# Performance work log

Measured on AMD Instinct MI355X. Metric: run time of the kernel, lower is better.

Reference implementation:

```python
import jax, jax.numpy as jnp
import numpy as np

ALPHA = 8.3  # depth-similarity decay from Depth-aware CNN
K = 3        # kernel size
PAD = 1      # padding (stride=1, dilation=1)


def _patches(x, k, pad):
    """Extract kxk stride-1 patches. x: (B,C,H,W) -> (B,C,k,k,H,W)."""
    B, C, H, W = x.shape
    xp = jnp.pad(x, ((0, 0), (0, 0), (pad, pad), (pad, pad)))
    rows = []
    for i in range(k):
        cols = [xp[:, :, i:i + H, j:j + W] for j in range(k)]
        rows.append(jnp.stack(cols, axis=2))          # (B,C,k,H,W)
    return jnp.stack(rows, axis=2)                     # (B,C,k,k,H,W)


def setup_inputs() -> dict:
    key = jax.random.key(0)
    k1, k2, k3 = jax.random.split(key, 3)
    B, Cin, H, W = 8, 512, 64, 64
    Cout = 64
    x = jax.random.normal(k1, (B, Cin, H, W), dtype=jnp.float32)
    depth = jax.random.uniform(k2, (B, 1, H, W), dtype=jnp.float32)
    stdv = 1.0 / np.sqrt(Cin * K * K)
    weight = jax.random.uniform(k3, (Cout, Cin, K, K), dtype=jnp.float32,
                                minval=-stdv, maxval=stdv)
    return {"input": x, "depth": depth, "weight": weight}


def reference(input, depth, weight):
    # depth-modulated conv: out(p0) = sum_pn w(pn) * x(p0+pn) * exp(-a*|d(p0)-d(p0+pn)|)
    xpat = _patches(input, K, PAD)                 # (B,Cin,K,K,H,W)
    dpat = _patches(depth, K, PAD)                 # (B,1,K,K,H,W)
    d0 = depth[:, :, None, None, :, :]             # center depth (B,1,1,1,H,W)
    gate = jnp.exp(-ALPHA * jnp.abs(d0 - dpat))    # (B,1,K,K,H,W)
    out = jnp.einsum('ocij,bcijhw->bohw', weight, xpat * gate)
    return out
```

## Files before the change

kernel.cpp:

```cpp
#include <hip/hip_runtime.h>
#include <math.h>

#define ALPHA 8.3f
#define XSZ   8448
#define WSZ   18432
#define BUFSZ 26880

typedef short v8s  __attribute__((ext_vector_type(8)));
typedef float v16f __attribute__((ext_vector_type(16)));
typedef float v4f  __attribute__((ext_vector_type(4)));

static __device__ __forceinline__ unsigned short f2bf(float f) {
    unsigned int u = __float_as_uint(f);
    u = (u + 0x7fffu + ((u >> 16) & 1u)) >> 16;
    return (unsigned short)u;
}

static __device__ __forceinline__ void async16(const void* g, void* l) {
    __builtin_amdgcn_global_load_lds(
        (const __attribute__((address_space(1))) unsigned int*)g,
        (__attribute__((address_space(3))) unsigned int*)l, 16, 0, 0);
}

__global__ void prep_weights(const float* __restrict__ w, unsigned short* __restrict__ wt,
                             float* __restrict__ zb) {
    if (blockIdx.x == 0) zb[threadIdx.x] = 0.f;
    int i = blockIdx.x * 256 + threadIdx.x;
    if (i >= 294912) return;
    int j    = i & 7;
    int lane = (i >> 3) & 63;
    int F    = i >> 9;
    int mt   = F & 1;
    int t    = F >> 1;
    int tap  = t % 9;
    int ss   = t / 9;
    int o   = mt * 32 + (lane & 31);
    int cin = ss * 16 + (lane >> 5) * 8 + j;
    wt[i] = f2bf(w[(o * 512 + cin) * 9 + tap]);
}

__global__ __launch_bounds__(256) void nhwc_cast(const float* __restrict__ x,
                                                 unsigned short* __restrict__ x2) {
    __shared__ float st[64][65];
    const int bx = blockIdx.x;
    const int cq = bx & 7;
    const int h  = (bx >> 3) & 63;
    const int b  = bx >> 9;
    const int tid = threadIdx.x;
    const float* xb = x + ((size_t)b * 512 + cq * 64) * 4096 + h * 64;
    unsigned short* ob = x2 + (((size_t)b * 64 + h) * 64) * 512 + cq * 64;
#pragma unroll
    for (int i = 0; i < 4; ++i) {
        const int c  = i * 16 + (tid >> 4);
        const int w4 = (tid & 15) * 4;
        const float4 v = *(const float4*)&xb[(size_t)c * 4096 + w4];
        st[c][w4]     = v.x;
        st[c][w4 + 1] = v.y;
        st[c][w4 + 2] = v.z;
        st[c][w4 + 3] = v.w;
    }
    __syncthreads();
#pragma unroll
    for (int j = 0; j < 2; ++j) {
        const int idx = j * 256 + tid;
        const int w = idx >> 3, k = idx & 7;
        unsigned short t[8];
#pragma unroll
        for (int e = 0; e < 8; ++e) t[e] = f2bf(st[k * 8 + e][w]);
        uint4 u;
        u.x = t[0] | ((unsigned)t[1] << 16);
        u.y = t[2] | ((unsigned)t[3] << 16);
        u.z = t[4] | ((unsigned)t[5] << 16);
        u.w = t[6] | ((unsigned)t[7] << 16);
        *(uint4*)&ob[(size_t)w * 512 + k * 8] = u;
    }
}

__global__ __launch_bounds__(384, 2)
void depthconv_v11(const unsigned short* __restrict__ x2,
                   const float* __restrict__ depth,
                   const unsigned short* __restrict__ wt,
                   const float* __restrict__ zbuf,
                   float* __restrict__ out) {
    __shared__ __align__(16) char smem[2 * BUFSZ];

    const int bx   = blockIdx.x;
    const int xcd  = bx & 7;
    const int i0   = bx >> 3;
    const int b    = i0 & 7;
    const int h0   = (xcd * 4 + (i0 >> 3)) * 2;

    const int tid  = threadIdx.x;
    const int wid  = tid >> 6;
    const int lane = tid & 63;
    const int l31  = lane & 31;
    const int half = lane >> 5;
    const int rt   = wid & 1;
    const int di   = wid >> 1;

    const char* xpix = (const char*)(x2 + ((size_t)b * 4096) * 512);

    const char* p0;
    const char* p1;
    {
        const int i_0 = tid;
        const int g_0 = (i_0 >= 264) ? 1 : 0;
        const int s_0 = i_0 - g_0 * 264;
        const int r_0 = s_0 / 66, c_0 = s_0 - r_0 * 66;
        const int hh0 = h0 - 1 + r_0, ww0 = c_0 - 1;
        p0 = (hh0 >= 0 && hh0 < 64 && ww0 >= 0 && ww0 < 64)
                 ? xpix + (size_t)(hh0 * 64 + ww0) * 1024 + g_0 * 16
                 : (const char*)zbuf;
        const int i_1 = 384 + tid;
        const int g_1 = (i_1 >= 264) ? 1 : 0;
        const int s_1 = i_1 - g_1 * 264;
        const int r_1 = s_1 / 66, c_1 = s_1 - r_1 * 66;
        const int hh1 = h0 - 1 + r_1, ww1 = c_1 - 1;
        p1 = (hh1 >= 0 && hh1 < 64 && ww1 >= 0 && ww1 < 64)
                 ? xpix + (size_t)(hh1 * 64 + ww1) * 1024 + g_1 * 16
                 : (const char*)zbuf;
    }
    const char* wsrc = (const char*)wt;

#define ISSUE(BSEL)                                                              \
    {                                                                            \
        char* dst = smem + (BSEL) * BUFSZ;                                       \
        async16(wsrc + (size_t)tid * 16,         dst + XSZ + tid * 16);          \
        async16(wsrc + (size_t)(384 + tid) * 16, dst + XSZ + (384 + tid) * 16);  \
        async16(wsrc + (size_t)(768 + tid) * 16, dst + XSZ + (768 + tid) * 16);  \
        async16(p0, dst + tid * 16);                                             \
        if (tid < 144) async16(p1, dst + (384 + tid) * 16);                      \
        p0 += 32; p1 += 32; wsrc += 18432;                                       \
    }

    ISSUE(0);

    float gt[2][3];
    {
        const float* dp = depth + (size_t)b * 4096;
        const int hq = h0 + rt;
        const int hn = hq + di - 1;
#pragma unroll
        for (int n = 0; n < 2; ++n) {
            const int wq = n * 32 + l31;
            const float d0 = dp[hq * 64 + wq];
#pragma unroll
            for (int dj = 0; dj < 3; ++dj) {
                const int wn = wq + dj - 1;
                const float dn = (hn >= 0 && hn < 64 && wn >= 0 && wn < 64)
                                     ? dp[hn * 64 + wn] : 0.f;
                gt[n][dj] = __expf(-ALPHA * fabsf(d0 - dn));
            }
        }
    }

    v16f a00[3], a01[3], a10[3], a11[3];
#pragma unroll
    for (int d = 0; d < 3; ++d)
#pragma unroll
        for (int r = 0; r < 16; ++r) { a00[d][r] = 0.f; a01[d][r] = 0.f;
                                       a10[d][r] = 0.f; a11[d][r] = 0.f; }

    const int aOff = XSZ + di * 6144 + lane * 16;
    const int bOff = (half * 264 + (rt + di) * 66 + l31) * 16;

    for (int ss = 0; ss < 32; ++ss) {
        __syncthreads();
        const int cur = ss & 1;
        if (ss < 31) ISSUE(cur ^ 1);
        const char* ba = smem + cur * BUFSZ + aOff;
        const char* bb = smem + cur * BUFSZ + bOff;
#pragma unroll
        for (int dj = 0; dj < 3; ++dj) {
            const v8s w0 = *(const v8s*)(ba + (dj * 2 + 0) * 1024);
            const v8s w1 = *(const v8s*)(ba + (dj * 2 + 1) * 1024);
            const v8s x0 = *(const v8s*)(bb + (0 * 32 + dj) * 16);
            const v8s x1 = *(const v8s*)(bb + (1 * 32 + dj) * 16);
            a00[dj] = __builtin_amdgcn_mfma_f32_32x32x16_bf16(w0, x0, a00[dj], 0, 0, 0);
            a01[dj] = __builtin_amdgcn_mfma_f32_32x32x16_bf16(w1, x0, a01[dj], 0, 0, 0);
            a10[dj] = __builtin_amdgcn_mfma_f32_32x32x16_bf16(w0, x1, a10[dj], 0, 0, 0);
            a11[dj] = __builtin_amdgcn_mfma_f32_32x32x16_bf16(w1, x1, a11[dj], 0, 0, 0);
        }
    }

#pragma unroll
    for (int r = 0; r < 16; ++r) {
        a00[0][r] = gt[0][0] * a00[0][r];
        a00[0][r] = fmaf(gt[0][1], a00[1][r], a00[0][r]);
        a00[0][r] = fmaf(gt[0][2], a00[2][r], a00[0][r]);
        a01[0][r] = gt[0][0] * a01[0][r];
        a01[0][r] = fmaf(gt[0][1], a01[1][r], a01[0][r]);
        a01[0][r] = fmaf(gt[0][2], a01[2][r], a01[0][r]);
        a10[0][r] = gt[1][0] * a10[0][r];
        a10[0][r] = fmaf(gt[1][1], a10[1][r], a10[0][r]);
        a10[0][r] = fmaf(gt[1][2], a10[2][r], a10[0][r]);
        a11[0][r] = gt[1][0] * a11[0][r];
        a11[0][r] = fmaf(gt[1][1], a11[1][r], a11[0][r]);
        a11[0][r] = fmaf(gt[1][2], a11[2][r], a11[0][r]);
    }

    __syncthreads();
    float* red = (float*)smem;
    const int rbase = rt * 4096 + lane * 4;
#define EPI_STORE(ACC, N, MT)                                                    \
    _Pragma("unroll")                                                            \
    for (int qd = 0; qd < 4; ++qd) {                                             \
        v4f v; v[0] = ACC[0][qd * 4]; v[1] = ACC[0][qd * 4 + 1];                 \
        v[2] = ACC[0][qd * 4 + 2]; v[3] = ACC[0][qd * 4 + 3];                    \
        *(v4f*)&red[rbase + ((N) * 2 + (MT)) * 1024 + qd * 256] = v;             \
    }
#define EPI_ADD(ACC, N, MT)                                                      \
    _Pragma("unroll")                                                            \
    for (int qd = 0; qd < 4; ++qd) {                                             \
        v4f v = *(const v4f*)&red[rbase + ((N) * 2 + (MT)) * 1024 + qd * 256];   \
        v[0] += ACC[0][qd * 4];     v[1] += ACC[0][qd * 4 + 1];                  \
        v[2] += ACC[0][qd * 4 + 2]; v[3] += ACC[0][qd * 4 + 3];                  \
        *(v4f*)&red[rbase + ((N) * 2 + (MT)) * 1024 + qd * 256] = v;             \
    }
    if (di == 2) {
        EPI_STORE(a00, 0, 0) EPI_STORE(a01, 0, 1) EPI_STORE(a10, 1, 0) EPI_STORE(a11, 1, 1)
    }
    __syncthreads();
    if (di == 1) {
        EPI_ADD(a00, 0, 0) EPI_ADD(a01, 0, 1) EPI_ADD(a10, 1, 0) EPI_ADD(a11, 1, 1)
    }
    __syncthreads();
    if (di == 0) {
        float* ob = out + (size_t)b * 262144 + (h0 + rt) * 64;
#define EPI_OUT(ACC, N, MT)                                                      \
    _Pragma("unroll")                                                            \
    for (int qd = 0; qd < 4; ++qd) {                                             \
        const v4f v = *(const v4f*)&red[rbase + ((N) * 2 + (MT)) * 1024 + qd * 256]; \
        _Pragma("unroll")                                                        \
        for (int j = 0; j < 4; ++j) {                                            \
            const int rg = qd * 4 + j;                                           \
            const int o = (MT) * 32 + (rg & 3) + 8 * (rg >> 2) + 4 * half;       \
            ob[(size_t)o * 4096 + (N) * 32 + l31] = ACC[0][rg] + v[j];           \
        }                                                                        \
    }
        EPI_OUT(a00, 0, 0) EPI_OUT(a01, 0, 1) EPI_OUT(a10, 1, 0) EPI_OUT(a11, 1, 1)
    }
}

extern "C" void kernel_launch(void* const* d_in, const int* in_sizes, int n_in,
                              void* d_out, int out_size, void* d_ws, size_t ws_size,
                              hipStream_t stream) {
    const float* x      = (const float*)d_in[0];
    const float* depth  = (const float*)d_in[1];
    const float* weight = (const float*)d_in[2];
    float* out = (float*)d_out;

    unsigned short* wtb = (unsigned short*)d_ws;
    float* zbuf         = (float*)((char*)d_ws + 786432);
    unsigned short* x2  = (unsigned short*)((char*)d_ws + (1 << 20));

    prep_weights<<<1152, 256, 0, stream>>>(weight, wtb, zbuf);
    nhwc_cast<<<4096, 256, 0, stream>>>(x, x2);
    depthconv_v11<<<256, 384, 0, stream>>>(x2, depth, wtb, zbuf, out);
}
```

Baseline: 132.5 us.

## Double the K-chunk per pipeline stage and merge prep kernels into one launch

The main conv loop now stages 32 input channels per double-buffered step instead of 16, halving the number of iterations and barriers. Each stage issues more async global-to-LDS loads and runs twice as many MFMAs per barrier. The weight reorder layout is changed to match the new chunking. Weight prep and the NHWC bf16 cast are fused into a single launch to remove one kernel launch. The cost is double the LDS footprint, about 105KB per block, which fits only one block per CU; the 256-block grid already places about one block per CU.

```diff
diff --git a/kernel.cpp b/kernel.cpp
--- a/kernel.cpp
+++ b/kernel.cpp
@@ -2,9 +2,9 @@
 #include <math.h>
 
 #define ALPHA 8.3f
-#define XSZ   8448
-#define WSZ   18432
-#define BUFSZ 26880
+#define XSZ   16896
+#define WSZ   36864
+#define BUFSZ 53760
 
 typedef short v8s  __attribute__((ext_vector_type(8)));
 typedef float v16f __attribute__((ext_vector_type(16)));
@@ -22,31 +22,33 @@
         (__attribute__((address_space(3))) unsigned int*)l, 16, 0, 0);
 }
 
-__global__ void prep_weights(const float* __restrict__ w, unsigned short* __restrict__ wt,
-                             float* __restrict__ zb) {
-    if (blockIdx.x == 0) zb[threadIdx.x] = 0.f;
-    int i = blockIdx.x * 256 + threadIdx.x;
-    if (i >= 294912) return;
-    int j    = i & 7;
-    int lane = (i >> 3) & 63;
-    int F    = i >> 9;
-    int mt   = F & 1;
-    int t    = F >> 1;
-    int tap  = t % 9;
-    int ss   = t / 9;
-    int o   = mt * 32 + (lane & 31);
-    int cin = ss * 16 + (lane >> 5) * 8 + j;
-    wt[i] = f2bf(w[(o * 512 + cin) * 9 + tap]);
-}
-
-__global__ __launch_bounds__(256) void nhwc_cast(const float* __restrict__ x,
-                                                 unsigned short* __restrict__ x2) {
+__global__ __launch_bounds__(256) void prep_and_cast(const float* __restrict__ x,
+                                                     unsigned short* __restrict__ x2,
+                                                     const float* __restrict__ w,
+                                                     unsigned short* __restrict__ wt,
+                                                     float* __restrict__ zb) {
     __shared__ float st[64][65];
-    const int bx = blockIdx.x;
+    const int bx  = blockIdx.x;
+    const int tid = threadIdx.x;
+    if (bx >= 4096) {
+        if (bx == 4096) zb[tid] = 0.f;
+        const int i = (bx - 4096) * 256 + tid;
+        const int j    = i & 7;
+        const int lane = (i >> 3) & 63;
+        const int F    = i >> 9;
+        const int kc   = F & 1;
+        const int mt   = (F >> 1) & 1;
+        const int tq   = F >> 2;
+        const int tap  = tq % 9;
+        const int ss   = tq / 9;
+        const int o    = mt * 32 + (lane & 31);
+        const int cin  = ss * 32 + kc * 16 + (lane >> 5) * 8 + j;
+        wt[i] = f2bf(w[(o * 512 + cin) * 9 + tap]);
+        return;
+    }
     const int cq = bx & 7;
     const int h  = (bx >> 3) & 63;
     const int b  = bx >> 9;
-    const int tid = threadIdx.x;
     const float* xb = x + ((size_t)b * 512 + cq * 64) * 4096 + h * 64;
     unsigned short* ob = x2 + (((size_t)b * 64 + h) * 64) * 512 + cq * 64;
 #pragma unroll
@@ -63,21 +65,21 @@
 #pragma unroll
     for (int j = 0; j < 2; ++j) {
         const int idx = j * 256 + tid;
-        const int w = idx >> 3, k = idx & 7;
+        const int ww = idx >> 3, k = idx & 7;
         unsigned short t[8];
 #pragma unroll
-        for (int e = 0; e < 8; ++e) t[e] = f2bf(st[k * 8 + e][w]);
+        for (int e = 0; e < 8; ++e) t[e] = f2bf(st[k * 8 + e][ww]);
         uint4 u;
         u.x = t[0] | ((unsigned)t[1] << 16);
         u.y = t[2] | ((unsigned)t[3] << 16);
         u.z = t[4] | ((unsigned)t[5] << 16);
         u.w = t[6] | ((unsigned)t[7] << 16);
-        *(uint4*)&ob[(size_t)w * 512 + k * 8] = u;
+        *(uint4*)&ob[(size_t)ww * 512 + k * 8] = u;
     }
 }
 
 __global__ __launch_bounds__(384, 2)
-void depthconv_v11(const unsigned short* __restrict__ x2,
+void depthconv_v12(const unsigned short* __restrict__ x2,
                    const float* __restrict__ depth,
                    const unsigned short* __restrict__ wt,
                    const float* __restrict__ zbuf,
@@ -100,37 +102,33 @@
 
     const char* xpix = (const char*)(x2 + ((size_t)b * 4096) * 512);
 
-    const char* p0;
-    const char* p1;
-    {
-        const int i_0 = tid;
-        const int g_0 = (i_0 >= 264) ? 1 : 0;
-        const int s_0 = i_0 - g_0 * 264;
-        const int r_0 = s_0 / 66, c_0 = s_0 - r_0 * 66;
-        const int hh0 = h0 - 1 + r_0, ww0 = c_0 - 1;
-        p0 = (hh0 >= 0 && hh0 < 64 && ww0 >= 0 && ww0 < 64)
-                 ? xpix + (size_t)(hh0 * 64 + ww0) * 1024 + g_0 * 16
-                 : (const char*)zbuf;
-        const int i_1 = 384 + tid;
-        const int g_1 = (i_1 >= 264) ? 1 : 0;
-        const int s_1 = i_1 - g_1 * 264;
-        const int r_1 = s_1 / 66, c_1 = s_1 - r_1 * 66;
-        const int hh1 = h0 - 1 + r_1, ww1 = c_1 - 1;
-        p1 = (hh1 >= 0 && hh1 < 64 && ww1 >= 0 && ww1 < 64)
-                 ? xpix + (size_t)(hh1 * 64 + ww1) * 1024 + g_1 * 16
-                 : (const char*)zbuf;
-    }
+    const char* p0; const char* p1; const char* p2;
+#define MKPTR(P, I)                                                              \
+    {                                                                            \
+        const int g_ = (I) / 264;                                                \
+        const int s_ = (I) - g_ * 264;                                           \
+        const int r_ = s_ / 66, c_ = s_ - r_ * 66;                               \
+        const int hh = h0 - 1 + r_, ww = c_ - 1;                                 \
+        P = (hh >= 0 && hh < 64 && ww >= 0 && ww < 64)                           \
+                ? xpix + (size_t)(hh * 64 + ww) * 1024 + g_ * 16                 \
+                : (const char*)zbuf;                                             \
+    }
+    MKPTR(p0, tid)
+    MKPTR(p1, 384 + tid)
+    MKPTR(p2, 768 + tid)
     const char* wsrc = (const char*)wt;
 
 #define ISSUE(BSEL)                                                              \
     {                                                                            \
         char* dst = smem + (BSEL) * BUFSZ;                                       \
-        async16(wsrc + (size_t)tid * 16,         dst + XSZ + tid * 16);          \
-        async16(wsrc + (size_t)(384 + tid) * 16, dst + XSZ + (384 + tid) * 16);  \
-        async16(wsrc + (size_t)(768 + tid) * 16, dst + XSZ + (768 + tid) * 16);  \
+        _Pragma("unroll")                                                        \
+        for (int k = 0; k < 6; ++k)                                              \
+            async16(wsrc + (size_t)(k * 384 + tid) * 16,                         \
+                    dst + XSZ + (k * 384 + tid) * 16);                           \
         async16(p0, dst + tid * 16);                                             \
-        if (tid < 144) async16(p1, dst + (384 + tid) * 16);                      \
-        p0 += 32; p1 += 32; wsrc += 18432;                                       \
+        async16(p1, dst + (384 + tid) * 16);                                     \
+        if (tid < 288) async16(p2, dst + (768 + tid) * 16);                      \
+        p0 += 64; p1 += 64; p2 += 64; wsrc += WSZ;                               \
     }
 
     ISSUE(0);
@@ -161,25 +159,28 @@
         for (int r = 0; r < 16; ++r) { a00[d][r] = 0.f; a01[d][r] = 0.f;
                                        a10[d][r] = 0.f; a11[d][r] = 0.f; }
 
-    const int aOff = XSZ + di * 6144 + lane * 16;
+    const int aOff = XSZ + di * 12288 + lane * 16;
     const int bOff = (half * 264 + (rt + di) * 66 + l31) * 16;
 
-    for (int ss = 0; ss < 32; ++ss) {
+    for (int ss = 0; ss < 16; ++ss) {
         __syncthreads();
         const int cur = ss & 1;
-        if (ss < 31) ISSUE(cur ^ 1);
+        if (ss < 15) ISSUE(cur ^ 1);
         const char* ba = smem + cur * BUFSZ + aOff;
         const char* bb = smem + cur * BUFSZ + bOff;
 #pragma unroll
         for (int dj = 0; dj < 3; ++dj) {
-            const v8s w0 = *(const v8s*)(ba + (dj * 2 + 0) * 1024);
-            const v8s w1 = *(const v8s*)(ba + (dj * 2 + 1) * 1024);
-            const v8s x0 = *(const v8s*)(bb + (0 * 32 + dj) * 16);
-            const v8s x1 = *(const v8s*)(bb + (1 * 32 + dj) * 16);
-            a00[dj] = __builtin_amdgcn_mfma_f32_32x32x16_bf16(w0, x0, a00[dj], 0, 0, 0);
-            a01[dj] = __builtin_amdgcn_mfma_f32_32x32x16_bf16(w1, x0, a01[dj], 0, 0, 0);
-            a10[dj] = __builtin_amdgcn_mfma_f32_32x32x16_bf16(w0, x1, a10[dj], 0, 0, 0);
-            a11[dj] = __builtin_amdgcn_mfma_f32_32x32x16_bf16(w1, x1, a11[dj], 0, 0, 0);
+#pragma unroll
+            for (int kc = 0; kc < 2; ++kc) {
+                const v8s w0 = *(const v8s*)(ba + ((dj * 2 + 0) * 2 + kc) * 1024);
+                const v8s w1 = *(const v8s*)(ba + ((dj * 2 + 1) * 2 + kc) * 1024);
+                const v8s x0 = *(const v8s*)(bb + kc * 8448 + (0 * 32 + dj) * 16);
+                const v8s x1 = *(const v8s*)(bb + kc * 8448 + (1 * 32 + dj) * 16);
+                a00[dj] = __builtin_amdgcn_mfma_f32_32x32x16_bf16(w0, x0, a00[dj], 0, 0, 0);
+                a01[dj] = __builtin_amdgcn_mfma_f32_32x32x16_bf16(w1, x0, a01[dj], 0, 0, 0);
+                a10[dj] = __builtin_amdgcn_mfma_f32_32x32x16_bf16(w0, x1, a10[dj], 0, 0, 0);
+                a11[dj] = __builtin_amdgcn_mfma_f32_32x32x16_bf16(w1, x1, a11[dj], 0, 0, 0);
+            }
         }
     }
 
@@ -254,7 +255,6 @@
     float* zbuf         = (float*)((char*)d_ws + 786432);
     unsigned short* x2  = (unsigned short*)((char*)d_ws + (1 << 20));
 
-    prep_weights<<<1152, 256, 0, stream>>>(weight, wtb, zbuf);
-    nhwc_cast<<<4096, 256, 0, stream>>>(x, x2);
-    depthconv_v11<<<256, 384, 0, stream>>>(x2, depth, wtb, zbuf, out);
-}
+    prep_and_cast<<<5248, 256, 0, stream>>>(x, x2, weight, wtb, zbuf);
+    depthconv_v12<<<256, 384, 0, stream>>>(x2, depth, wtb, zbuf, out);
+}
```

Measured after the change: 127.8 us. 3.6% less time.
